# Kernel optimization log

Measured on AMD Instinct MI355X. Metric: run time of the kernel, lower is better.

Reference implementation:

```python
import jax, jax.numpy as jnp
import numpy as np

TOP_K = 2
EPS = 1e-6

def setup_inputs() -> dict:
    key = jax.random.key(0)
    ks = jax.random.split(key, 4)
    B, L, D, E, ED = 2, 2048, 2048, 8, 2048
    scale_gu = (6.0 / D) ** 0.5   # kaiming_uniform-ish bound
    scale_dn = (6.0 / ED) ** 0.5
    return {
        "x": jax.random.normal(ks[0], (B, L, D), jnp.float32),
        "router_scale": jnp.ones((D,), jnp.float32),
        "gate_w": jax.random.normal(ks[1], (D, E), jnp.float32) * (D ** -0.5),
        "gate_up": jax.random.uniform(ks[2], (E, D, 2 * ED), jnp.float32, -scale_gu, scale_gu),
        "down": jax.random.uniform(ks[3], (E, ED, D), jnp.float32, -scale_dn, scale_dn),
        "per_expert_scale": jnp.ones((E,), jnp.float32),
    }

def reference(x, router_scale, gate_w, gate_up, down, per_expert_scale):
    B, L, D = x.shape
    E = gate_up.shape[0]
    # --- Router: RMSNorm (no scale) * D^-0.5 * router_scale -> linear -> softmax -> topk -> renorm
    h = x * jax.lax.rsqrt(jnp.mean(x * x, axis=-1, keepdims=True) + EPS)
    h = h * (D ** -0.5) * router_scale
    logits = (h @ gate_w).astype(jnp.float32)            # [B,L,E]
    probs = jax.nn.softmax(logits, axis=-1)
    w, idx = jax.lax.top_k(probs, TOP_K)                 # [B,L,K]
    w = w / jnp.clip(jnp.sum(w, axis=-1, keepdims=True), 1e-12)
    w = w.astype(x.dtype)
    # --- Experts: dense compute over all experts, weighted combine by routing
    N = B * L
    xf = x.reshape(N, D)
    idxf = idx.reshape(N, TOP_K)
    wf = w.reshape(N, TOP_K)
    # combine[n,e] = sum_k wf[n,k] * (idxf[n,k]==e); top_k indices are distinct per token
    combine = jnp.zeros((N, E), x.dtype).at[jnp.arange(N)[:, None], idxf].add(wf)
    hh = jnp.einsum('nd,edf->nef', xf, gate_up)          # [N,E,2*ED]
    gate, up = jnp.split(hh, 2, axis=-1)
    act = jax.nn.gelu(gate, approximate=False) * up      # [N,E,ED]
    y = jnp.einsum('nef,efd->ned', act, down)            # [N,E,D]
    out = jnp.einsum('ne,ned->nd', combine * per_expert_scale, y)
    return out.reshape(B, L, D)
```

## Files before the change

kernel.cpp:

```cpp
#include <hip/hip_runtime.h>
#include <hip/hip_bf16.h>
#include <math.h>

#define NTOK 4096
#define DM   2048
#define NE   8
#define BK   64

using f32x4  = float __attribute__((ext_vector_type(4)));
using bf16x8 = __bf16 __attribute__((ext_vector_type(8)));
using u32x4  = unsigned int __attribute__((ext_vector_type(4)));

__device__ __forceinline__ unsigned short bf16bits(float f){
  unsigned u = __builtin_bit_cast(unsigned, f);
  return (unsigned short)((u + 0x7fffu + ((u >> 16) & 1u)) >> 16);
}

__device__ __forceinline__ float bfhi(unsigned u){ return __builtin_bit_cast(float, u & 0xffff0000u); }
__device__ __forceinline__ float bflo(unsigned u){ return __builtin_bit_cast(float, u << 16); }

__device__ __forceinline__ void load_lds16(const void* g, void* l){
  __builtin_amdgcn_global_load_lds(
      (const __attribute__((address_space(1))) unsigned int*)g,
      (__attribute__((address_space(3))) unsigned int*)l, 16, 0, 0);
}

__global__ __launch_bounds__(256) void router_kernel(
    const float* __restrict__ x, const float* __restrict__ rs,
    const float* __restrict__ gw, const float* __restrict__ pes,
    unsigned short* __restrict__ xbf, int* __restrict__ cnt,
    int* __restrict__ toklist, float* __restrict__ slotw)
{
  const int wv = threadIdx.x >> 6, l = threadIdx.x & 63;
  const int n = blockIdx.x * 4 + wv;
  const float* xr = x + (size_t)n * DM;
  unsigned short* xb = xbf + (size_t)n * DM;
  float ssq = 0.f;
  float lg[8] = {0,0,0,0,0,0,0,0};
  #pragma unroll
  for (int q = 0; q < 8; ++q){
    int c4 = l + 64 * q;
    float4 v = ((const float4*)xr)[c4];
    float4 r = ((const float4*)rs)[c4];
    ssq += v.x*v.x + v.y*v.y + v.z*v.z + v.w*v.w;
    ushort4 o; o.x = bf16bits(v.x); o.y = bf16bits(v.y); o.z = bf16bits(v.z); o.w = bf16bits(v.w);
    ((ushort4*)xb)[c4] = o;
    float xs0 = v.x*r.x, xs1 = v.y*r.y, xs2 = v.z*r.z, xs3 = v.w*r.w;
    const float4* gp = (const float4*)(gw + (size_t)c4 * 32);
    float4 ga, gb;
    ga = gp[0]; gb = gp[1];
    lg[0]+=xs0*ga.x; lg[1]+=xs0*ga.y; lg[2]+=xs0*ga.z; lg[3]+=xs0*ga.w;
    lg[4]+=xs0*gb.x; lg[5]+=xs0*gb.y; lg[6]+=xs0*gb.z; lg[7]+=xs0*gb.w;
    ga = gp[2]; gb = gp[3];
    lg[0]+=xs1*ga.x; lg[1]+=xs1*ga.y; lg[2]+=xs1*ga.z; lg[3]+=xs1*ga.w;
    lg[4]+=xs1*gb.x; lg[5]+=xs1*gb.y; lg[6]+=xs1*gb.z; lg[7]+=xs1*gb.w;
    ga = gp[4]; gb = gp[5];
    lg[0]+=xs2*ga.x; lg[1]+=xs2*ga.y; lg[2]+=xs2*ga.z; lg[3]+=xs2*ga.w;
    lg[4]+=xs2*gb.x; lg[5]+=xs2*gb.y; lg[6]+=xs2*gb.z; lg[7]+=xs2*gb.w;
    ga = gp[6]; gb = gp[7];
    lg[0]+=xs3*ga.x; lg[1]+=xs3*ga.y; lg[2]+=xs3*ga.z; lg[3]+=xs3*ga.w;
    lg[4]+=xs3*gb.x; lg[5]+=xs3*gb.y; lg[6]+=xs3*gb.z; lg[7]+=xs3*gb.w;
  }
  #pragma unroll
  for (int off = 32; off; off >>= 1){
    ssq += __shfl_xor(ssq, off, 64);
    #pragma unroll
    for (int e2 = 0; e2 < 8; ++e2) lg[e2] += __shfl_xor(lg[e2], off, 64);
  }
  if (l == 0){
    float c = rsqrtf(ssq * (1.0f/DM) + 1e-6f) * 0.022097086912079608f;
    float mx = -1e30f;
    #pragma unroll
    for (int e2 = 0; e2 < 8; ++e2){ lg[e2] *= c; mx = fmaxf(mx, lg[e2]); }
    float l0 = lg[0]; int i0 = 0;
    #pragma unroll
    for (int e2 = 1; e2 < 8; ++e2) if (lg[e2] > l0){ l0 = lg[e2]; i0 = e2; }
    int i1 = (i0 == 0) ? 1 : 0; float l1 = (i0 == 0) ? lg[1] : lg[0];
    #pragma unroll
    for (int e2 = 0; e2 < 8; ++e2){ if (e2 != i0 && lg[e2] > l1){ l1 = lg[e2]; i1 = e2; } }
    float p0 = expf(l0 - mx), p1 = expf(l1 - mx);
    float sw = fmaxf(p0 + p1, 1e-12f);
    float w0 = p0 / sw, w1 = p1 / sw;
    int s0 = atomicAdd(&cnt[i0], 1);
    toklist[i0 * NTOK + s0] = n;
    slotw[i0 * NTOK + s0] = w0 * pes[i0];
    int s1 = atomicAdd(&cnt[i1], 1);
    toklist[i1 * NTOK + s1] = n;
    slotw[i1 * NTOK + s1] = w1 * pes[i1];
  }
}

__global__ void scan_kernel(const int* __restrict__ cnt, int* __restrict__ basep){
  if (threadIdx.x == 0){
    int a = 0;
    for (int e = 0; e < NE; ++e){ basep[e] = a; a += cnt[e]; }
  }
}

__global__ __launch_bounds__(256) void conv_transpose_kernel(
    const float* __restrict__ W, unsigned short* __restrict__ Wt, int ncols)
{
  const int z = blockIdx.z;
  const float* src = W + (size_t)z * 2048 * ncols;
  unsigned short* dst = Wt + (size_t)z * ncols * 2048;
  const int n0 = blockIdx.x * 64, k0 = blockIdx.y * 64;
  __shared__ __align__(16) unsigned short t[64][72];
  const int tid = threadIdx.x;
  const int kl = tid >> 4;
  const int nl = (tid & 15) * 4;
  #pragma unroll
  for (int q = 0; q < 4; ++q){
    int k = kl + q * 16;
    float4 v = *(const float4*)(src + (size_t)(k0 + k) * ncols + n0 + nl);
    t[nl+0][k] = bf16bits(v.x);
    t[nl+1][k] = bf16bits(v.y);
    t[nl+2][k] = bf16bits(v.z);
    t[nl+3][k] = bf16bits(v.w);
  }
  __syncthreads();
  const int nr = tid >> 3;
  const int k8 = (tid & 7) * 8;
  #pragma unroll
  for (int q = 0; q < 2; ++q){
    int n = nr + q * 32;
    u32x4 v = *(const u32x4*)&t[n][k8];
    *(u32x4*)(dst + (size_t)(n0 + n) * 2048 + k0 + k8) = v;
  }
}

template<int MODE>
__global__ __launch_bounds__(256, 4) void moe_gemm(
    const unsigned short* __restrict__ Abuf,
    const unsigned short* __restrict__ Wt,
    unsigned short* __restrict__ hh,
    float* __restrict__ out,
    const int* __restrict__ cnt,
    const int* __restrict__ basep,
    const int* __restrict__ toklist,
    const float* __restrict__ slotw,
    int e0)
{
  const int z = blockIdx.z, e = e0 + z;
  const int ce = cnt[e];
  const int m0 = blockIdx.y * 128;
  if (m0 >= ce) return;
  const int fb = blockIdx.x * 128;
  const int tid = threadIdx.x;
  const int l = tid & 63;
  const int wv = tid >> 6;
  const int wr = wv >> 1, wc = wv & 1;
  const int baseE = basep[e];
  const size_t ncols = (MODE == 0) ? 4096 : 2048;
  const unsigned short* Wz = Wt + (size_t)z * ncols * 2048;

  __shared__ __align__(16) unsigned short As[128 * BK];
  __shared__ __align__(16) unsigned short Bs[128 * BK];

  const unsigned short* asrc[4];
  const unsigned short* bsrc[4];
  #pragma unroll
  for (int q = 0; q < 4; ++q){
    int row = q * 32 + (tid >> 3);
    int g = (tid & 7) ^ (row & 7);
    long rs;
    if (MODE == 0) rs = toklist[e * NTOK + min(m0 + row, ce - 1)];
    else           rs = baseE + min(m0 + row, ce - 1);
    asrc[q] = Abuf + (size_t)rs * 2048 + g * 8;
    bsrc[q] = Wz + (size_t)(fb + row) * 2048 + g * 8;
  }

  f32x4 acc[4][4];
  #pragma unroll
  for (int i = 0; i < 4; ++i)
    #pragma unroll
    for (int j = 0; j < 4; ++j)
      acc[i][j] = (f32x4){0.f, 0.f, 0.f, 0.f};

  const int aoff0 = (wr * 64 + (l & 15)) * BK;
  const int boff0 = (wc * 64 + (l & 15)) * BK;
  const int lsw = l & 7;
  const int lq = l >> 4;

  #pragma unroll 1
  for (int k0 = 0; k0 < 2048; k0 += BK){
    if (k0) __syncthreads();
    #pragma unroll
    for (int q = 0; q < 4; ++q)
      load_lds16(asrc[q] + k0, &As[q * 2048 + wv * 512]);
    #pragma unroll
    for (int q = 0; q < 4; ++q)
      load_lds16(bsrc[q] + k0, &Bs[q * 2048 + wv * 512]);
    __syncthreads();
    #pragma unroll
    for (int kk = 0; kk < 2; ++kk){
      const int gsw = ((kk * 4 + lq) ^ lsw) * 8;
      bf16x8 af[4];
      #pragma unroll
      for (int mi = 0; mi < 4; ++mi)
        af[mi] = *(const bf16x8*)&As[aoff0 + mi * 16 * BK + gsw];
      #pragma unroll
      for (int ni = 0; ni < 4; ++ni){
        bf16x8 bfr = *(const bf16x8*)&Bs[boff0 + ni * 16 * BK + gsw];
        #pragma unroll
        for (int mi = 0; mi < 4; ++mi)
          acc[mi][ni] = __builtin_amdgcn_mfma_f32_16x16x32_bf16(
              af[mi], bfr, acc[mi][ni], 0, 0, 0);
      }
    }
  }

  const int lq4 = (l >> 4) * 4;
  if (MODE == 0){
    const int fcol = fb + wc * 64 + (l & 15);
    #pragma unroll
    for (int mi = 0; mi < 4; ++mi)
      #pragma unroll
      for (int j = 0; j < 4; ++j){
        int s = m0 + wr * 64 + mi * 16 + lq4 + j;
        if (s < ce){
          size_t rowb = (size_t)(baseE + s) * 4096 + fcol;
          #pragma unroll
          for (int ni = 0; ni < 4; ++ni)
            hh[rowb + ni * 16] = bf16bits(acc[mi][ni][j]);
        }
      }
  } else {
    #pragma unroll
    for (int mi = 0; mi < 4; ++mi)
      #pragma unroll
      for (int j = 0; j < 4; ++j){
        int s = m0 + wr * 64 + mi * 16 + lq4 + j;
        if (s < ce){
          int tokn = toklist[e * NTOK + s];
          float wgt = slotw[e * NTOK + s];
          float* orow = out + (size_t)tokn * 2048 + fb + wc * 64 + (l & 15);
          #pragma unroll
          for (int ni = 0; ni < 4; ++ni)
            atomicAdd(&orow[ni * 16], wgt * acc[mi][ni][j]);
        }
      }
  }
}

__global__ __launch_bounds__(256) void gelu_mul_kernel(
    const unsigned short* __restrict__ hh, unsigned short* __restrict__ act)
{
  const int s = blockIdx.x;
  const int t = threadIdx.x;
  const unsigned short* gp = hh + (size_t)s * 4096 + t * 8;
  u32x4 gv = *(const u32x4*)gp;
  u32x4 uv = *(const u32x4*)(gp + 2048);
  unsigned short r[8];
  #pragma unroll
  for (int i = 0; i < 4; ++i){
    float g0 = bflo(gv[i]), g1 = bfhi(gv[i]);
    float u0 = bflo(uv[i]), u1 = bfhi(uv[i]);
    float a0 = 0.5f * g0 * (1.0f + erff(g0 * 0.70710678118654752f)) * u0;
    float a1 = 0.5f * g1 * (1.0f + erff(g1 * 0.70710678118654752f)) * u1;
    r[2*i]   = bf16bits(a0);
    r[2*i+1] = bf16bits(a1);
  }
  *(u32x4*)(act + (size_t)s * 2048 + t * 8) = *(u32x4*)r;
}

extern "C" void kernel_launch(void* const* d_in, const int* in_sizes, int n_in,
                              void* d_out, int out_size, void* d_ws, size_t ws_size,
                              hipStream_t stream)
{
  const float* x   = (const float*)d_in[0];
  const float* rs  = (const float*)d_in[1];
  const float* gw  = (const float*)d_in[2];
  const float* w1  = (const float*)d_in[3];
  const float* w2  = (const float*)d_in[4];
  const float* pes = (const float*)d_in[5];
  float* out = (float*)d_out;

  char* ws = (char*)d_ws;
  int*   cnt      = (int*)ws;
  int*   basep    = (int*)(ws + 64);
  int*   toklist  = (int*)(ws + 256);
  float* slotw    = (float*)(ws + 256 + (size_t)NE * NTOK * 4);
  unsigned short* xbf  = (unsigned short*)(ws + 256 + 2 * (size_t)NE * NTOK * 4);
  unsigned short* act  = xbf + (size_t)NTOK * DM;
  unsigned short* hh   = act + (size_t)2 * NTOK * DM;
  unsigned short* wtb  = hh + (size_t)2 * NTOK * 4096;

  const size_t fixed = (size_t)((char*)wtb - ws);
  const size_t per_e = (size_t)4096 * 2048 * 2;
  int EG = (int)((ws_size > fixed) ? ((ws_size - fixed) / per_e) : 0);
  if (EG < 1) EG = 1;
  if (EG > NE) EG = NE;

  hipMemsetAsync(out, 0, (size_t)out_size * sizeof(float), stream);
  hipMemsetAsync(cnt, 0, 64, stream);
  router_kernel<<<NTOK / 4, 256, 0, stream>>>(x, rs, gw, pes, xbf, cnt, toklist, slotw);
  scan_kernel<<<1, 64, 0, stream>>>(cnt, basep);

  for (int g = 0; g < NE; g += EG){
    int gg = min(EG, NE - g);
    conv_transpose_kernel<<<dim3(64, 32, gg), 256, 0, stream>>>(
        w1 + (size_t)g * 2048 * 4096, wtb, 4096);
    moe_gemm<0><<<dim3(32, 32, gg), 256, 0, stream>>>(
        xbf, wtb, hh, out, cnt, basep, toklist, slotw, g);
  }
  gelu_mul_kernel<<<2 * NTOK, 256, 0, stream>>>(hh, act);
  for (int g = 0; g < NE; g += EG){
    int gg = min(EG, NE - g);
    conv_transpose_kernel<<<dim3(32, 32, gg), 256, 0, stream>>>(
        w2 + (size_t)g * 2048 * 2048, wtb, 2048);
    moe_gemm<1><<<dim3(16, 32, gg), 256, 0, stream>>>(
        act, wtb, hh, out, cnt, basep, toklist, slotw, g);
  }
}
```

Baseline: 527.6 us.

## Fuse GELU-multiply into gate/up GEMM epilogue and swizzle block order

Each gate/up GEMM tile now loads 64 gate columns and the matching 64 up columns, so the epilogue computes gelu(gate)*up and writes activations directly. This removes the intermediate hh buffer and the separate gelu kernel, and with them a round trip of the large intermediate through memory. Blocks are also remapped to a flat 1D index that groups 4 M-tiles per column tile, which should improve weight reuse in cache. The output tile width per GEMM drops from 128 to 64 activation columns, and more of the epilogue is erf math.

```diff
diff --git a/kernel.cpp b/kernel.cpp
--- a/kernel.cpp
+++ b/kernel.cpp
@@ -15,9 +15,6 @@
   unsigned u = __builtin_bit_cast(unsigned, f);
   return (unsigned short)((u + 0x7fffu + ((u >> 16) & 1u)) >> 16);
 }
-
-__device__ __forceinline__ float bfhi(unsigned u){ return __builtin_bit_cast(float, u & 0xffff0000u); }
-__device__ __forceinline__ float bflo(unsigned u){ return __builtin_bit_cast(float, u << 16); }
 
 __device__ __forceinline__ void load_lds16(const void* g, void* l){
   __builtin_amdgcn_global_load_lds(
@@ -132,7 +129,7 @@
 __global__ __launch_bounds__(256, 4) void moe_gemm(
     const unsigned short* __restrict__ Abuf,
     const unsigned short* __restrict__ Wt,
-    unsigned short* __restrict__ hh,
+    unsigned short* __restrict__ act,
     float* __restrict__ out,
     const int* __restrict__ cnt,
     const int* __restrict__ basep,
@@ -142,9 +139,12 @@
 {
   const int z = blockIdx.z, e = e0 + z;
   const int ce = cnt[e];
-  const int m0 = blockIdx.y * 128;
+  const int flat = blockIdx.x;
+  int mc, rr, fbi, m0;
+  if (MODE == 0){ mc = flat >> 7; rr = flat & 127; fbi = rr >> 2; }
+  else          { mc = flat >> 6; rr = flat & 63;  fbi = rr >> 2; }
+  m0 = ((mc << 2) + (rr & 3)) << 7;
   if (m0 >= ce) return;
-  const int fb = blockIdx.x * 128;
   const int tid = threadIdx.x;
   const int l = tid & 63;
   const int wv = tid >> 6;
@@ -166,7 +166,10 @@
     if (MODE == 0) rs = toklist[e * NTOK + min(m0 + row, ce - 1)];
     else           rs = baseE + min(m0 + row, ce - 1);
     asrc[q] = Abuf + (size_t)rs * 2048 + g * 8;
-    bsrc[q] = Wz + (size_t)(fb + row) * 2048 + g * 8;
+    int wcol;
+    if (MODE == 0) wcol = (row < 64) ? (fbi * 64 + row) : (2048 + fbi * 64 + row - 64);
+    else           wcol = fbi * 128 + row;
+    bsrc[q] = Wz + (size_t)wcol * 2048 + g * 8;
   }
 
   f32x4 acc[4][4];
@@ -177,7 +180,16 @@
       acc[i][j] = (f32x4){0.f, 0.f, 0.f, 0.f};
 
   const int aoff0 = (wr * 64 + (l & 15)) * BK;
-  const int boff0 = (wc * 64 + (l & 15)) * BK;
+  int boffs[4];
+  if (MODE == 0){
+    boffs[0] = (wc * 32 + (l & 15)) * BK;
+    boffs[1] = (wc * 32 + 16 + (l & 15)) * BK;
+    boffs[2] = (64 + wc * 32 + (l & 15)) * BK;
+    boffs[3] = (64 + wc * 32 + 16 + (l & 15)) * BK;
+  } else {
+    #pragma unroll
+    for (int ni = 0; ni < 4; ++ni) boffs[ni] = (wc * 64 + ni * 16 + (l & 15)) * BK;
+  }
   const int lsw = l & 7;
   const int lq = l >> 4;
 
@@ -200,7 +212,7 @@
         af[mi] = *(const bf16x8*)&As[aoff0 + mi * 16 * BK + gsw];
       #pragma unroll
       for (int ni = 0; ni < 4; ++ni){
-        bf16x8 bfr = *(const bf16x8*)&Bs[boff0 + ni * 16 * BK + gsw];
+        bf16x8 bfr = *(const bf16x8*)&Bs[boffs[ni] + gsw];
         #pragma unroll
         for (int mi = 0; mi < 4; ++mi)
           acc[mi][ni] = __builtin_amdgcn_mfma_f32_16x16x32_bf16(
@@ -211,17 +223,20 @@
 
   const int lq4 = (l >> 4) * 4;
   if (MODE == 0){
-    const int fcol = fb + wc * 64 + (l & 15);
     #pragma unroll
     for (int mi = 0; mi < 4; ++mi)
       #pragma unroll
       for (int j = 0; j < 4; ++j){
         int s = m0 + wr * 64 + mi * 16 + lq4 + j;
         if (s < ce){
-          size_t rowb = (size_t)(baseE + s) * 4096 + fcol;
+          size_t rowb = (size_t)(baseE + s) * 2048;
           #pragma unroll
-          for (int ni = 0; ni < 4; ++ni)
-            hh[rowb + ni * 16] = bf16bits(acc[mi][ni][j]);
+          for (int p = 0; p < 2; ++p){
+            float g = acc[mi][p][j];
+            float u = acc[mi][p + 2][j];
+            float a = 0.5f * g * (1.0f + erff(g * 0.70710678118654752f)) * u;
+            act[rowb + fbi * 64 + wc * 32 + p * 16 + (l & 15)] = bf16bits(a);
+          }
         }
       }
   } else {
@@ -233,34 +248,13 @@
         if (s < ce){
           int tokn = toklist[e * NTOK + s];
           float wgt = slotw[e * NTOK + s];
-          float* orow = out + (size_t)tokn * 2048 + fb + wc * 64 + (l & 15);
+          float* orow = out + (size_t)tokn * 2048 + fbi * 128 + wc * 64 + (l & 15);
           #pragma unroll
           for (int ni = 0; ni < 4; ++ni)
             atomicAdd(&orow[ni * 16], wgt * acc[mi][ni][j]);
         }
       }
   }
-}
-
-__global__ __launch_bounds__(256) void gelu_mul_kernel(
-    const unsigned short* __restrict__ hh, unsigned short* __restrict__ act)
-{
-  const int s = blockIdx.x;
-  const int t = threadIdx.x;
-  const unsigned short* gp = hh + (size_t)s * 4096 + t * 8;
-  u32x4 gv = *(const u32x4*)gp;
-  u32x4 uv = *(const u32x4*)(gp + 2048);
-  unsigned short r[8];
-  #pragma unroll
-  for (int i = 0; i < 4; ++i){
-    float g0 = bflo(gv[i]), g1 = bfhi(gv[i]);
-    float u0 = bflo(uv[i]), u1 = bfhi(uv[i]);
-    float a0 = 0.5f * g0 * (1.0f + erff(g0 * 0.70710678118654752f)) * u0;
-    float a1 = 0.5f * g1 * (1.0f + erff(g1 * 0.70710678118654752f)) * u1;
-    r[2*i]   = bf16bits(a0);
-    r[2*i+1] = bf16bits(a1);
-  }
-  *(u32x4*)(act + (size_t)s * 2048 + t * 8) = *(u32x4*)r;
 }
 
 extern "C" void kernel_launch(void* const* d_in, const int* in_sizes, int n_in,
@@ -282,33 +276,40 @@
   float* slotw    = (float*)(ws + 256 + (size_t)NE * NTOK * 4);
   unsigned short* xbf  = (unsigned short*)(ws + 256 + 2 * (size_t)NE * NTOK * 4);
   unsigned short* act  = xbf + (size_t)NTOK * DM;
-  unsigned short* hh   = act + (size_t)2 * NTOK * DM;
-  unsigned short* wtb  = hh + (size_t)2 * NTOK * 4096;
+  unsigned short* wtb  = act + (size_t)2 * NTOK * DM;
 
   const size_t fixed = (size_t)((char*)wtb - ws);
   const size_t per_e = (size_t)4096 * 2048 * 2;
-  int EG = (int)((ws_size > fixed) ? ((ws_size - fixed) / per_e) : 0);
-  if (EG < 1) EG = 1;
-  if (EG > NE) EG = NE;
 
   hipMemsetAsync(out, 0, (size_t)out_size * sizeof(float), stream);
   hipMemsetAsync(cnt, 0, 64, stream);
   router_kernel<<<NTOK / 4, 256, 0, stream>>>(x, rs, gw, pes, xbf, cnt, toklist, slotw);
   scan_kernel<<<1, 64, 0, stream>>>(cnt, basep);
 
-  for (int g = 0; g < NE; g += EG){
-    int gg = min(EG, NE - g);
-    conv_transpose_kernel<<<dim3(64, 32, gg), 256, 0, stream>>>(
-        w1 + (size_t)g * 2048 * 4096, wtb, 4096);
-    moe_gemm<0><<<dim3(32, 32, gg), 256, 0, stream>>>(
-        xbf, wtb, hh, out, cnt, basep, toklist, slotw, g);
-  }
-  gelu_mul_kernel<<<2 * NTOK, 256, 0, stream>>>(hh, act);
-  for (int g = 0; g < NE; g += EG){
-    int gg = min(EG, NE - g);
-    conv_transpose_kernel<<<dim3(32, 32, gg), 256, 0, stream>>>(
-        w2 + (size_t)g * 2048 * 2048, wtb, 2048);
-    moe_gemm<1><<<dim3(16, 32, gg), 256, 0, stream>>>(
-        act, wtb, hh, out, cnt, basep, toklist, slotw, g);
-  }
-}
+  if (ws_size >= fixed + (size_t)NE * per_e){
+    conv_transpose_kernel<<<dim3(64, 32, NE), 256, 0, stream>>>(w1, wtb, 4096);
+    moe_gemm<0><<<dim3(1024, 1, NE), 256, 0, stream>>>(
+        xbf, wtb, act, out, cnt, basep, toklist, slotw, 0);
+    conv_transpose_kernel<<<dim3(32, 32, NE), 256, 0, stream>>>(w2, wtb, 2048);
+    moe_gemm<1><<<dim3(512, 1, NE), 256, 0, stream>>>(
+        act, wtb, act, out, cnt, basep, toklist, slotw, 0);
+  } else {
+    int EG = (int)((ws_size > fixed) ? ((ws_size - fixed) / per_e) : 0);
+    if (EG < 1) EG = 1;
+    if (EG > NE) EG = NE;
+    for (int g = 0; g < NE; g += EG){
+      int gg = min(EG, NE - g);
+      conv_transpose_kernel<<<dim3(64, 32, gg), 256, 0, stream>>>(
+          w1 + (size_t)g * 2048 * 4096, wtb, 4096);
+      moe_gemm<0><<<dim3(1024, 1, gg), 256, 0, stream>>>(
+          xbf, wtb, act, out, cnt, basep, toklist, slotw, g);
+    }
+    for (int g = 0; g < NE; g += EG){
+      int gg = min(EG, NE - g);
+      conv_transpose_kernel<<<dim3(32, 32, gg), 256, 0, stream>>>(
+          w2 + (size_t)g * 2048 * 2048, wtb, 2048);
+      moe_gemm<1><<<dim3(512, 1, gg), 256, 0, stream>>>(
+          act, wtb, act, out, cnt, basep, toklist, slotw, g);
+    }
+  }
+}
```

Result: slower. 558.2 us (+5.8%).
